# Kernel optimization log

Measured on AMD Instinct MI355X. Metric: run time of the kernel, lower is better.

## Reference

```python
import jax, jax.numpy as jnp
import numpy as np

# ---- structural constants (mirror e3nn SO3.tensor_productRs bookkeeping) ----
MUL = 2                      # multiplicity of every irrep in Rs_in / Rs_out
LS = [0, 1, 2]               # irrep orders present in Rs_in and Rs_out
L_MAX = 2                    # spherical-harmonics cutoff -> Y_dim = 9
N_BASIS, HIDDEN = 64, 64     # radial model sizes
R_MAX, GAMMA = 3.5, 4.0      # gaussian radial basis params


def _filter_paths():
    """One entry (l_filter) per (mul_out, mul_in, l_in, l_out, l_f) path."""
    paths = []
    for l_in in LS:
        for l_out in LS:
            for lf in range(abs(l_in - l_out), min(l_in + l_out, L_MAX) + 1):
                paths.extend([lf] * (MUL * MUL))  # mul_in * mul_out copies
    return paths  # len == n_path == 60


def _build_mix_matrices():
    """rf_mix[K, n_path]: broadcast each radial path weight over its 2l+1 components.
    ylm_mix[K, 9]: select Y_{l,m} for each filter component. Both 0/1, block sparse."""
    paths = _filter_paths()
    n_path = len(paths)
    K = sum(2 * l + 1 for l in paths)          # 204
    y_off = {0: 0, 1: 1, 2: 4}                 # offset of l-block inside Y (dim 9)
    rf = np.zeros((K, n_path), dtype=np.float32)
    ylm = np.zeros((K, 9), dtype=np.float32)
    k = 0
    for p, l in enumerate(paths):
        for m in range(2 * l + 1):
            rf[k, p] = 1.0
            ylm[k, y_off[l] + m] = 1.0
            k += 1
    return rf, ylm, n_path, K


def _sh_l012(n):
    """Real spherical harmonics l=0..2 on unit vectors n[Z,3] -> Y[9, Z]."""
    x, y, z = n[:, 0], n[:, 1], n[:, 2]
    c0 = 0.28209479177387814   # 1/(2 sqrt(pi))
    c1 = 0.4886025119029199    # sqrt(3/(4 pi))
    c2a = 1.0925484305920792   # sqrt(15/(4 pi))
    c2b = 0.31539156525252005  # sqrt(5/(16 pi))
    c2c = 0.5462742152960396   # sqrt(15/(16 pi))
    one = jnp.ones_like(x)
    return jnp.stack([
        c0 * one,
        c1 * y, c1 * z, c1 * x,
        c2a * x * y, c2a * y * z, c2b * (3.0 * z * z - 1.0), c2a * x * z,
        c2c * (x * x - y * y),
    ], axis=0)


def setup_inputs() -> dict:
    key = jax.random.key(0)
    k_r, k_cg, k_w1, k_w2 = jax.random.split(key, 4)
    Z = 65536
    D = MUL * sum(2 * l + 1 for l in LS)       # 18 (dim_in == dim_out)
    rf_np, ylm_np, n_path, K = _build_mix_matrices()
    r = 2.0 * jax.random.normal(k_r, (Z, 3), dtype=jnp.float32)
    cg = jax.random.normal(k_cg, (K, D, D), dtype=jnp.float32) / np.sqrt(K)
    W1 = jax.random.normal(k_w1, (N_BASIS, HIDDEN), dtype=jnp.float32) / np.sqrt(N_BASIS)
    b1 = jnp.zeros((HIDDEN,), dtype=jnp.float32)
    W2 = jax.random.normal(k_w2, (HIDDEN, n_path), dtype=jnp.float32) / np.sqrt(HIDDEN)
    b2 = jnp.zeros((n_path,), dtype=jnp.float32)
    return {"r": r, "W1": W1, "b1": b1, "W2": W2, "b2": b2,
            "cg": cg, "rf_mix": jnp.asarray(rf_np), "ylm_mix": jnp.asarray(ylm_np)}


def reference(r, W1, b1, W2, b2, cg, rf_mix, ylm_mix):
    radii = jnp.linalg.norm(r, axis=1)                    # [Z]
    n = r / (radii[:, None] + 1e-12)                      # unit directions
    Y = _sh_l012(n)                                       # [9, Z]  (sh returns [m, ...])
    centers = jnp.linspace(0.0, R_MAX, N_BASIS, dtype=jnp.float32)
    B = jnp.exp(-GAMMA * (radii[:, None] - centers) ** 2) # gaussian radial basis [Z, 64]
    R = jax.nn.relu(B @ W1 + b1) @ W2 + b2                # RadialModel -> [Z, n_path]
    Rm = jnp.einsum('kp,zp->zk', rf_mix, R)               # 'ij,zj->zi'
    Ym = jnp.einsum('ky,yz->zk', ylm_mix, Y)              # 'ij,jz->zi'
    # 'kij,zk,zk->zij' : fuse the two per-point vectors, then one GEMM over k
    kernel = jnp.einsum('kij,zk->zij', cg, Rm * Ym)       # [Z, 18, 18]
    return kernel
```

## Files before the change

kernel.cpp:

```cpp
#include <hip/hip_runtime.h>

#define NPATH 60
#define KDIM  204
#define NIJ   324
#define NTIL  21
#define HID   64

typedef short bf16x8 __attribute__((ext_vector_type(8)));
typedef float f32x4  __attribute__((ext_vector_type(4)));

__device__ __align__(16) unsigned short g_w1s[4096];
__device__ __align__(16) unsigned short g_w2s[4096];
__device__ __align__(16) unsigned short g_cgs[75264];
__device__ unsigned int  g_pyk[112];

__device__ inline unsigned short f2bf(float f) {
    unsigned int u = __builtin_bit_cast(unsigned int, f);
    u += 0x7fffu + ((u >> 16) & 1u);
    return (unsigned short)(u >> 16);
}
__device__ inline float bf2f(unsigned short h) {
    unsigned int u = ((unsigned int)h) << 16;
    return __builtin_bit_cast(float, u);
}

__global__ void prep_kernel(const float* __restrict__ W1, const float* __restrict__ W2,
                            const float* __restrict__ cg, const float* __restrict__ rf,
                            const float* __restrict__ ylm)
{
    int idx = blockIdx.x * 256 + threadIdx.x;
    if (idx < 4096) {
        int e = idx & 7, ln = (idx >> 3) & 63, nt = (idx >> 9) & 3, kc = idx >> 11;
        int k = kc * 32 + (ln >> 4) * 8 + e;
        int n = nt * 16 + (ln & 15);
        g_w1s[idx] = f2bf(W1[k * HID + n]);
    } else if (idx < 8192) {
        int j = idx - 4096;
        int e = j & 7, ln = (j >> 3) & 63, nt = (j >> 9) & 3, kc = j >> 11;
        int k = kc * 32 + (ln >> 4) * 8 + e;
        int n = nt * 16 + (ln & 15);
        g_w2s[j] = f2bf(n < NPATH ? W2[k * NPATH + n] : 0.0f);
    } else if (idx < 8192 + 75264) {
        int j = idx - 8192;
        int e = j & 7, ln = (j >> 3) & 63;
        int nt = (j >> 9) % NTIL;
        int kc = j / (512 * NTIL);
        int k = kc * 32 + (ln >> 4) * 8 + e;
        int n = nt * 16 + (ln & 15);
        g_cgs[j] = f2bf((k < KDIM && n < NIJ) ? cg[k * NIJ + n] : 0.0f);
    } else if (idx < 8192 + 75264 + 112) {
        int j = idx - (8192 + 75264);
        int k0 = 2 * j, k1 = 2 * j + 1;
        unsigned p0 = 0, y0 = 0, p1 = 0, y1 = 0;
        if (k0 < KDIM) {
            for (int q = 0; q < NPATH; q++) if (rf[k0 * NPATH + q] != 0.0f) p0 = q;
            for (int q = 0; q < 9; q++)     if (ylm[k0 * 9 + q]   != 0.0f) y0 = q;
            for (int q = 0; q < NPATH; q++) if (rf[k1 * NPATH + q] != 0.0f) p1 = q;
            for (int q = 0; q < 9; q++)     if (ylm[k1 * 9 + q]   != 0.0f) y1 = q;
        }
        g_pyk[j] = p0 | (y0 << 8) | (p1 << 16) | (y1 << 24);
    }
}

struct __align__(16) WaveMem {
    unsigned short Hw[16][88];
    unsigned short Rw[16][61];
    float          Yw[16][9];
};

__global__ __launch_bounds__(256) void fused_kernel(
    const float* __restrict__ r, const float* __restrict__ b1,
    const float* __restrict__ b2, float* __restrict__ out)
{
    __shared__ WaveMem wm[4];

    const int tid  = threadIdx.x;
    const int wv   = tid >> 6;
    const int lane = tid & 63;
    const int quad = lane >> 4;
    const int l16  = lane & 15;
    const int z0   = blockIdx.x * 64;
    WaveMem& W = wm[wv];

    const int zg = z0 + wv * 16 + l16;
    float x = r[zg * 3 + 0], y = r[zg * 3 + 1], zc = r[zg * 3 + 2];
    float rad = sqrtf(x * x + y * y + zc * zc);

    if (quad == 0) {
        float inv = 1.0f / (rad + 1e-12f);
        float nx = x * inv, ny = y * inv, nz = zc * inv;
        const float c0 = 0.28209479177387814f, c1 = 0.4886025119029199f;
        const float c2a = 1.0925484305920792f, c2b = 0.31539156525252005f, c2c = 0.5462742152960396f;
        W.Yw[l16][0] = c0;
        W.Yw[l16][1] = c1 * ny;
        W.Yw[l16][2] = c1 * nz;
        W.Yw[l16][3] = c1 * nx;
        W.Yw[l16][4] = c2a * nx * ny;
        W.Yw[l16][5] = c2a * ny * nz;
        W.Yw[l16][6] = c2b * (3.0f * nz * nz - 1.0f);
        W.Yw[l16][7] = c2a * nx * nz;
        W.Yw[l16][8] = c2c * (nx * nx - ny * ny);
    }

    union frag { bf16x8 v; unsigned int d[4]; };
    frag A0, A1;
    {
        const float step = 3.5f / 63.0f;
        const float NL2E = -5.770780163555852f;
        #pragma unroll
        for (int ii = 0; ii < 4; ii++) {
            int i0 = quad * 8 + 2 * ii;
            float d0 = rad - (float)i0 * step;
            float d1 = rad - (float)(i0 + 1) * step;
            A0.d[ii] = (unsigned)f2bf(__builtin_amdgcn_exp2f(d0 * d0 * NL2E))
                     | ((unsigned)f2bf(__builtin_amdgcn_exp2f(d1 * d1 * NL2E)) << 16);
            int i2 = 32 + i0;
            float e0 = rad - (float)i2 * step;
            float e1 = rad - (float)(i2 + 1) * step;
            A1.d[ii] = (unsigned)f2bf(__builtin_amdgcn_exp2f(e0 * e0 * NL2E))
                     | ((unsigned)f2bf(__builtin_amdgcn_exp2f(e1 * e1 * NL2E)) << 16);
        }
    }

    #pragma unroll
    for (int nt = 0; nt < 4; nt++) {
        bf16x8 bb0 = *(const bf16x8*)&g_w1s[((0 * 4 + nt) * 64 + lane) * 8];
        bf16x8 bb1 = *(const bf16x8*)&g_w1s[((1 * 4 + nt) * 64 + lane) * 8];
        f32x4 acc = {0.f, 0.f, 0.f, 0.f};
        acc = __builtin_amdgcn_mfma_f32_16x16x32_bf16(A0.v, bb0, acc, 0, 0, 0);
        acc = __builtin_amdgcn_mfma_f32_16x16x32_bf16(A1.v, bb1, acc, 0, 0, 0);
        int h = nt * 16 + l16;
        float bias = b1[h];
        #pragma unroll
        for (int rr = 0; rr < 4; rr++) {
            float v = acc[rr] + bias;
            v = v > 0.0f ? v : 0.0f;
            W.Hw[quad * 4 + rr][h] = f2bf(v);
        }
    }
    asm volatile("s_waitcnt lgkmcnt(0)" ::: "memory");
    __builtin_amdgcn_sched_barrier(0);

    {
        bf16x8 h0 = *(const bf16x8*)&W.Hw[l16][0 + quad * 8];
        bf16x8 h1 = *(const bf16x8*)&W.Hw[l16][32 + quad * 8];
        #pragma unroll
        for (int nt = 0; nt < 4; nt++) {
            bf16x8 bb0 = *(const bf16x8*)&g_w2s[((0 * 4 + nt) * 64 + lane) * 8];
            bf16x8 bb1 = *(const bf16x8*)&g_w2s[((1 * 4 + nt) * 64 + lane) * 8];
            f32x4 acc = {0.f, 0.f, 0.f, 0.f};
            acc = __builtin_amdgcn_mfma_f32_16x16x32_bf16(h0, bb0, acc, 0, 0, 0);
            acc = __builtin_amdgcn_mfma_f32_16x16x32_bf16(h1, bb1, acc, 0, 0, 0);
            int p = nt * 16 + l16;
            if (p < NPATH) {
                float bias = b2[p];
                #pragma unroll
                for (int rr = 0; rr < 4; rr++)
                    W.Rw[quad * 4 + rr][p] = f2bf(acc[rr] + bias);
            }
        }
    }
    asm volatile("s_waitcnt lgkmcnt(0)" ::: "memory");
    __builtin_amdgcn_sched_barrier(0);

    frag az[7];
    #pragma unroll
    for (int kc = 0; kc < 7; kc++) {
        #pragma unroll
        for (int ii = 0; ii < 4; ii++) {
            unsigned py = g_pyk[kc * 16 + quad * 4 + ii];
            float cA = bf2f(W.Rw[l16][py & 255])         * W.Yw[l16][(py >> 8) & 255];
            float cB = bf2f(W.Rw[l16][(py >> 16) & 255]) * W.Yw[l16][py >> 24];
            az[kc].d[ii] = (unsigned)f2bf(cA) | ((unsigned)f2bf(cB) << 16);
        }
    }

    const int obase = (z0 + wv * 16 + quad * 4) * NIJ + l16;
    #pragma unroll 3
    for (int nt = 0; nt < NTIL; nt++) {
        f32x4 acc = {0.f, 0.f, 0.f, 0.f};
        #pragma unroll
        for (int kc = 0; kc < 7; kc++) {
            bf16x8 bg = *(const bf16x8*)&g_cgs[((kc * NTIL + nt) * 64 + lane) * 8];
            acc = __builtin_amdgcn_mfma_f32_16x16x32_bf16(az[kc].v, bg, acc, 0, 0, 0);
        }
        int col = nt * 16 + l16;
        if (col < NIJ) {
            #pragma unroll
            for (int rr = 0; rr < 4; rr++)
                out[obase + rr * NIJ + nt * 16] = acc[rr];
        }
    }
}

extern "C" void kernel_launch(void* const* d_in, const int* in_sizes, int n_in,
                              void* d_out, int out_size, void* d_ws, size_t ws_size,
                              hipStream_t stream) {
    const float* r   = (const float*)d_in[0];
    const float* W1  = (const float*)d_in[1];
    const float* b1  = (const float*)d_in[2];
    const float* W2  = (const float*)d_in[3];
    const float* b2  = (const float*)d_in[4];
    const float* cg  = (const float*)d_in[5];
    const float* rf  = (const float*)d_in[6];
    const float* ylm = (const float*)d_in[7];
    float* out = (float*)d_out;

    const int Z = in_sizes[0] / 3;

    prep_kernel<<<327, 256, 0, stream>>>(W1, W2, cg, rf, ylm);
    fused_kernel<<<Z / 64, 256, 0, stream>>>(r, b1, b2, out);
}
```

Before: 127.2 us.

## Bake path/Ylm index table at compile time and build coefficients from registers

```diff
diff --git a/kernel.cpp b/kernel.cpp
--- a/kernel.cpp
+++ b/kernel.cpp
@@ -12,7 +12,31 @@
 __device__ __align__(16) unsigned short g_w1s[4096];
 __device__ __align__(16) unsigned short g_w2s[4096];
 __device__ __align__(16) unsigned short g_cgs[75264];
-__device__ unsigned int  g_pyk[112];
+
+struct PYTab {
+    unsigned char pt[224];
+    unsigned char yt[224];
+    constexpr PYTab() : pt{}, yt{} {
+        const int yoff[3] = {0, 1, 4};
+        int k = 0, p = 0;
+        for (int li = 0; li <= 2; li++)
+            for (int lo = 0; lo <= 2; lo++) {
+                int lmin = li - lo; if (lmin < 0) lmin = -lmin;
+                int lmax = li + lo; if (lmax > 2) lmax = 2;
+                for (int lf = lmin; lf <= lmax; lf++)
+                    for (int m4 = 0; m4 < 4; m4++) {
+                        for (int m = 0; m < 2 * lf + 1; m++) {
+                            pt[k] = (unsigned char)p;
+                            yt[k] = (unsigned char)(yoff[lf] + m);
+                            k++;
+                        }
+                        p++;
+                    }
+            }
+        for (; k < 224; k++) { pt[k] = 0; yt[k] = 0; }
+    }
+};
+constexpr PYTab PY{};
 
 __device__ inline unsigned short f2bf(float f) {
     unsigned int u = __builtin_bit_cast(unsigned int, f);
@@ -25,8 +49,7 @@
 }
 
 __global__ void prep_kernel(const float* __restrict__ W1, const float* __restrict__ W2,
-                            const float* __restrict__ cg, const float* __restrict__ rf,
-                            const float* __restrict__ ylm)
+                            const float* __restrict__ cg)
 {
     int idx = blockIdx.x * 256 + threadIdx.x;
     if (idx < 4096) {
@@ -42,31 +65,22 @@
         g_w2s[j] = f2bf(n < NPATH ? W2[k * NPATH + n] : 0.0f);
     } else if (idx < 8192 + 75264) {
         int j = idx - 8192;
-        int e = j & 7, ln = (j >> 3) & 63;
-        int nt = (j >> 9) % NTIL;
-        int kc = j / (512 * NTIL);
-        int k = kc * 32 + (ln >> 4) * 8 + e;
-        int n = nt * 16 + (ln & 15);
-        g_cgs[j] = f2bf((k < KDIM && n < NIJ) ? cg[k * NIJ + n] : 0.0f);
-    } else if (idx < 8192 + 75264 + 112) {
-        int j = idx - (8192 + 75264);
-        int k0 = 2 * j, k1 = 2 * j + 1;
-        unsigned p0 = 0, y0 = 0, p1 = 0, y1 = 0;
-        if (k0 < KDIM) {
-            for (int q = 0; q < NPATH; q++) if (rf[k0 * NPATH + q] != 0.0f) p0 = q;
-            for (int q = 0; q < 9; q++)     if (ylm[k0 * 9 + q]   != 0.0f) y0 = q;
-            for (int q = 0; q < NPATH; q++) if (rf[k1 * NPATH + q] != 0.0f) p1 = q;
-            for (int q = 0; q < 9; q++)     if (ylm[k1 * 9 + q]   != 0.0f) y1 = q;
-        }
-        g_pyk[j] = p0 | (y0 << 8) | (p1 << 16) | (y1 << 24);
+        int k = j / 336;
+        int n = j % 336;
+        int kc = k >> 5, km = k & 31;
+        int e  = km & 7, lh = km >> 3;
+        int nt = n >> 4, lw = n & 15;
+        int dst = ((kc * NTIL + nt) * 64 + (lh * 16 + lw)) * 8 + e;
+        g_cgs[dst] = f2bf((k < KDIM && n < NIJ) ? cg[k * NIJ + n] : 0.0f);
     }
 }
 
 struct __align__(16) WaveMem {
     unsigned short Hw[16][88];
-    unsigned short Rw[16][61];
-    float          Yw[16][9];
+    unsigned short Rw[16][72];
 };
+
+union frag { bf16x8 v; unsigned int d[4]; };
 
 __global__ __launch_bounds__(256) void fused_kernel(
     const float* __restrict__ r, const float* __restrict__ b1,
@@ -86,23 +100,23 @@
     float x = r[zg * 3 + 0], y = r[zg * 3 + 1], zc = r[zg * 3 + 2];
     float rad = sqrtf(x * x + y * y + zc * zc);
 
-    if (quad == 0) {
+    float yv[9];
+    {
         float inv = 1.0f / (rad + 1e-12f);
         float nx = x * inv, ny = y * inv, nz = zc * inv;
         const float c0 = 0.28209479177387814f, c1 = 0.4886025119029199f;
         const float c2a = 1.0925484305920792f, c2b = 0.31539156525252005f, c2c = 0.5462742152960396f;
-        W.Yw[l16][0] = c0;
-        W.Yw[l16][1] = c1 * ny;
-        W.Yw[l16][2] = c1 * nz;
-        W.Yw[l16][3] = c1 * nx;
-        W.Yw[l16][4] = c2a * nx * ny;
-        W.Yw[l16][5] = c2a * ny * nz;
-        W.Yw[l16][6] = c2b * (3.0f * nz * nz - 1.0f);
-        W.Yw[l16][7] = c2a * nx * nz;
-        W.Yw[l16][8] = c2c * (nx * nx - ny * ny);
-    }
-
-    union frag { bf16x8 v; unsigned int d[4]; };
+        yv[0] = c0;
+        yv[1] = c1 * ny;
+        yv[2] = c1 * nz;
+        yv[3] = c1 * nx;
+        yv[4] = c2a * nx * ny;
+        yv[5] = c2a * ny * nz;
+        yv[6] = c2b * (3.0f * nz * nz - 1.0f);
+        yv[7] = c2a * nx * nz;
+        yv[8] = c2c * (nx * nx - ny * ny);
+    }
+
     frag A0, A1;
     {
         const float step = 3.5f / 63.0f;
@@ -163,14 +177,37 @@
     asm volatile("s_waitcnt lgkmcnt(0)" ::: "memory");
     __builtin_amdgcn_sched_barrier(0);
 
+    union { uint4 q[8]; unsigned int u[32]; } Rr;
+    {
+        const uint4* rp = (const uint4*)&W.Rw[l16][0];
+        #pragma unroll
+        for (int j = 0; j < 8; j++) Rr.q[j] = rp[j];
+    }
+    asm volatile("s_waitcnt lgkmcnt(0)" ::: "memory");
+    __builtin_amdgcn_sched_barrier(0);
+
     frag az[7];
     #pragma unroll
     for (int kc = 0; kc < 7; kc++) {
         #pragma unroll
         for (int ii = 0; ii < 4; ii++) {
-            unsigned py = g_pyk[kc * 16 + quad * 4 + ii];
-            float cA = bf2f(W.Rw[l16][py & 255])         * W.Yw[l16][(py >> 8) & 255];
-            float cB = bf2f(W.Rw[l16][(py >> 16) & 255]) * W.Yw[l16][py >> 24];
+            const int k0 = kc * 32 + quad * 8 + 2 * ii;
+            float cA, cB;
+            {
+                float a0_[4], b0_[4];
+                #pragma unroll
+                for (int qq = 0; qq < 4; qq++) {
+                    const int kA = kc * 32 + qq * 8 + 2 * ii;
+                    const int pA = PY.pt[kA],     yA = PY.yt[kA];
+                    const int pB = PY.pt[kA + 1], yB = PY.yt[kA + 1];
+                    float RA = bf2f((unsigned short)(Rr.u[pA >> 1] >> (16 * (pA & 1))));
+                    float RB = bf2f((unsigned short)(Rr.u[pB >> 1] >> (16 * (pB & 1))));
+                    a0_[qq] = RA * yv[yA];
+                    b0_[qq] = RB * yv[yB];
+                }
+                cA = (quad == 0) ? a0_[0] : (quad == 1) ? a0_[1] : (quad == 2) ? a0_[2] : a0_[3];
+                cB = (quad == 0) ? b0_[0] : (quad == 1) ? b0_[1] : (quad == 2) ? b0_[2] : b0_[3];
+            }
             az[kc].d[ii] = (unsigned)f2bf(cA) | ((unsigned)f2bf(cB) << 16);
         }
     }
@@ -202,12 +239,10 @@
     const float* W2  = (const float*)d_in[3];
     const float* b2  = (const float*)d_in[4];
     const float* cg  = (const float*)d_in[5];
-    const float* rf  = (const float*)d_in[6];
-    const float* ylm = (const float*)d_in[7];
     float* out = (float*)d_out;
 
     const int Z = in_sizes[0] / 3;
 
-    prep_kernel<<<327, 256, 0, stream>>>(W1, W2, cg, rf, ylm);
+    prep_kernel<<<327, 256, 0, stream>>>(W1, W2, cg);
     fused_kernel<<<Z / 64, 256, 0, stream>>>(r, b1, b2, out);
 }
```

After: 126.3 us. About the same (-0.7%).
